# Performance work log

Hardware: AMD Instinct MI355X
Metric: run time of the kernel (lower is better)

The kernel has to match this reference:

```python
import jax, jax.numpy as jnp
import numpy as np

B, T, C = 2, 2048, 1024
H = 16
D = C // H  # head_size = 64
FF = 4 * C
EPS = 1e-5


def _layernorm(x, g, b):
    mu = jnp.mean(x, axis=-1, keepdims=True)
    var = jnp.var(x, axis=-1, keepdims=True)
    return (x - mu) * jax.lax.rsqrt(var + EPS) * g + b


def setup_inputs() -> dict:
    key = jax.random.key(0)
    ks = jax.random.split(key, 12)
    s_in = 1.0 / np.sqrt(C)
    s_ff = 1.0 / np.sqrt(FF)
    return {
        "x": jax.random.normal(ks[0], (B, T, C), jnp.float32),
        "Wq": jax.random.uniform(ks[1], (H, C, D), jnp.float32, -s_in, s_in),
        "Wk": jax.random.uniform(ks[2], (H, C, D), jnp.float32, -s_in, s_in),
        "Wv": jax.random.uniform(ks[3], (H, C, D), jnp.float32, -s_in, s_in),
        "Wo": jax.random.uniform(ks[4], (C, C), jnp.float32, -s_in, s_in),
        "bo": jax.random.uniform(ks[5], (C,), jnp.float32, -s_in, s_in),
        "W1": jax.random.uniform(ks[6], (C, FF), jnp.float32, -s_in, s_in),
        "b1": jax.random.uniform(ks[7], (FF,), jnp.float32, -s_in, s_in),
        "W2": jax.random.uniform(ks[8], (FF, C), jnp.float32, -s_ff, s_ff),
        "b2": jax.random.uniform(ks[9], (C,), jnp.float32, -s_ff, s_ff),
        "g1": jnp.ones((C,), jnp.float32),
        "be1": jnp.zeros((C,), jnp.float32),
        "g2": jnp.ones((C,), jnp.float32),
        "be2": jnp.zeros((C,), jnp.float32),
    }


def reference(x, Wq, Wk, Wv, Wo, bo, W1, b1, W2, b2, g1, be1, g2, be2):
    h = _layernorm(x, g1, be1)
    # per-head projections (no bias), vectorized over heads
    q = jnp.einsum("btc,hcd->bhtd", h, Wq)
    k = jnp.einsum("btc,hcd->bhtd", h, Wk)
    v = jnp.einsum("btc,hcd->bhtd", h, Wv)
    # NOTE: original scales by n_embd**-0.5 (C, not head_size) -- faithful
    scores = jnp.einsum("bhtd,bhsd->bhts", q, k) * (C ** -0.5)
    causal = jnp.tril(jnp.ones((T, T), bool))
    scores = jnp.where(causal, scores, -jnp.inf)
    att = jax.nn.softmax(scores, axis=-1)
    out = jnp.einsum("bhts,bhsd->bhtd", att, v)
    out = out.transpose(0, 2, 1, 3).reshape(B, T, C)  # concat heads
    x = out @ Wo + bo + x  # attn residual (dropout=0 -> identity)
    h2 = _layernorm(x, g2, be2)
    ff = jax.nn.relu(h2 @ W1 + b1) @ W2 + b2
    return x + ff
```

## Files before the change

kernel.cpp:

```cpp
#include <hip/hip_runtime.h>
#include <stdint.h>

typedef unsigned short ushort_t;
typedef __attribute__((ext_vector_type(8))) short bf16x8;
typedef __attribute__((ext_vector_type(4))) float f32x4;

__device__ __forceinline__ unsigned short f2b(float f) {
  unsigned u = __float_as_uint(f);
  u += 0x7fffu + ((u >> 16) & 1u);
  return (unsigned short)(u >> 16);
}

__device__ __forceinline__ void async16(const void* g, void* l) {
  __builtin_amdgcn_global_load_lds(
      (const __attribute__((address_space(1))) void*)g,
      (__attribute__((address_space(3))) void*)l, 16, 0, 0);
}

__global__ __launch_bounds__(256) void ln_kernel(
    const float* __restrict__ x, const float* __restrict__ g,
    const float* __restrict__ be, ushort_t* __restrict__ out) {
  const int C = 1024;
  int row = blockIdx.x;
  const float4* xr = (const float4*)(x + (size_t)row * C);
  int tid = threadIdx.x;
  float4 v = xr[tid];
  float s = v.x + v.y + v.z + v.w;
  float sq = v.x * v.x + v.y * v.y + v.z * v.z + v.w * v.w;
  #pragma unroll
  for (int off = 32; off > 0; off >>= 1) {
    s += __shfl_xor(s, off);
    sq += __shfl_xor(sq, off);
  }
  __shared__ float ss[4], ssq[4];
  int wv = tid >> 6;
  if ((tid & 63) == 0) { ss[wv] = s; ssq[wv] = sq; }
  __syncthreads();
  s = ss[0] + ss[1] + ss[2] + ss[3];
  sq = ssq[0] + ssq[1] + ssq[2] + ssq[3];
  float mu = s * (1.f / C);
  float var = sq * (1.f / C) - mu * mu;
  float rs = rsqrtf(var + 1e-5f);
  float4 gv = ((const float4*)g)[tid];
  float4 bv = ((const float4*)be)[tid];
  ushort4 o;
  o.x = f2b((v.x - mu) * rs * gv.x + bv.x);
  o.y = f2b((v.y - mu) * rs * gv.y + bv.y);
  o.z = f2b((v.z - mu) * rs * gv.z + bv.z);
  o.w = f2b((v.w - mu) * rs * gv.w + bv.w);
  ((ushort4*)(out + (size_t)row * C))[tid] = o;
}

__global__ __launch_bounds__(256) void reduce2_kernel(
    const float* __restrict__ p0, const float* __restrict__ p1,
    const float* __restrict__ bias, const float* __restrict__ resid,
    float* __restrict__ out) {
  int idx = blockIdx.x * 256 + threadIdx.x;
  float4 a = ((const float4*)p0)[idx];
  float4 b = ((const float4*)p1)[idx];
  float4 r = ((const float4*)resid)[idx];
  float4 bi = ((const float4*)bias)[idx & 255];
  float4 o;
  o.x = a.x + b.x + r.x + bi.x;
  o.y = a.y + b.y + r.y + bi.y;
  o.z = a.z + b.z + r.z + bi.z;
  o.w = a.w + b.w + r.w + bi.w;
  ((float4*)out)[idx] = o;
}

__global__ __launch_bounds__(256) void transpose_cast_kernel(
    const float* __restrict__ in, ushort_t* __restrict__ out, int R, int Cin) {
  __shared__ float tile[32][33];
  int bz = blockIdx.z;
  in += (size_t)bz * R * Cin;
  out += (size_t)bz * R * Cin;
  int c0 = blockIdx.x * 32, r0 = blockIdx.y * 32;
  int tx = threadIdx.x, ty = threadIdx.y;
  #pragma unroll
  for (int i = 0; i < 4; i++)
    tile[ty + 8 * i][tx] = in[(size_t)(r0 + ty + 8 * i) * Cin + c0 + tx];
  __syncthreads();
  #pragma unroll
  for (int i = 0; i < 4; i++)
    out[(size_t)(c0 + ty + 8 * i) * R + r0 + tx] = f2b(tile[tx][ty + 8 * i]);
}

__global__ __launch_bounds__(256) void transpose_v_kernel(
    const ushort_t* __restrict__ qkv, ushort_t* __restrict__ vt) {
  __shared__ ushort_t tile[32][33];
  int bh = blockIdx.z;
  int b = bh >> 4, h = bh & 15;
  int d0 = blockIdx.x * 32, t0 = blockIdx.y * 32;
  int tx = threadIdx.x, ty = threadIdx.y;
  #pragma unroll
  for (int i = 0; i < 4; i++)
    tile[ty + 8 * i][tx] =
        qkv[(size_t)(b * 2048 + t0 + ty + 8 * i) * 3072 + 2048 + h * 64 + d0 + tx];
  __syncthreads();
  #pragma unroll
  for (int i = 0; i < 4; i++)
    vt[(size_t)(bh * 64 + d0 + ty + 8 * i) * 2048 + t0 + tx] = tile[tx][ty + 8 * i];
}

template <int BN, int N, int K, int FLAGS, int SK>
__global__ __launch_bounds__(256, 3) void gemm_bt_kernel(
    const ushort_t* __restrict__ A, const ushort_t* __restrict__ Bt,
    const float* __restrict__ bias, const float* __restrict__ resid,
    void* __restrict__ outv, float* __restrict__ pp0, float* __restrict__ pp1) {
  constexpr int KS = K / SK;
  __shared__ ushort_t Als[2][128 * 32];
  __shared__ ushort_t Bls[2][128 * 32];
  int tid = threadIdx.x, w = tid >> 6, lane = tid & 63, quad = lane >> 4, l16 = lane & 15;
  int fid = blockIdx.x;
  int bn_low = (fid >> 3) & 7;
  int meta = (fid & 7) | ((fid >> 6) << 3);
  int bm = meta & 31;
  int high = meta >> 5;
  int bn, zz;
  if constexpr (SK > 1) { zz = high; bn = bn_low; }
  else { zz = 0; bn = bn_low + 8 * high; }
  int bn0 = bn * 128, bm0 = bm * 128;
  int koff = (SK > 1) ? zz * KS : 0;
  int wm = (w >> 1) * 64, wn = (w & 1) * 64;
  f32x4 acc[4][4];
  #pragma unroll
  for (int i = 0; i < 4; i++)
    #pragma unroll
    for (int j = 0; j < 4; j++) acc[i][j] = f32x4{0.f, 0.f, 0.f, 0.f};
  const ushort_t* Ag = A + (size_t)bm0 * K + koff;
  const ushort_t* Bg = Bt + (size_t)bn0 * K + koff;
  int lr = lane >> 2, lco = (lane & 3) * 8;
  auto stage = [&](int k0, int bi) {
    async16(Ag + (size_t)(w * 32 + lr) * K + k0 + lco, &Als[bi][w * 1024]);
    async16(Ag + (size_t)(w * 32 + 16 + lr) * K + k0 + lco, &Als[bi][w * 1024 + 512]);
    async16(Bg + (size_t)(w * 32 + lr) * K + k0 + lco, &Bls[bi][w * 1024]);
    async16(Bg + (size_t)(w * 32 + 16 + lr) * K + k0 + lco, &Bls[bi][w * 1024 + 512]);
  };
  stage(0, 0);
  int s = 0;
  for (int k0 = 0; k0 < KS; k0 += 32, s ^= 1) {
    __syncthreads();
    if (k0 + 32 < KS) stage(k0 + 32, s ^ 1);
    bf16x8 af[4], bf[4];
    #pragma unroll
    for (int i = 0; i < 4; i++)
      af[i] = *(const bf16x8*)&Als[s][(wm + i * 16 + l16) * 32 + quad * 8];
    #pragma unroll
    for (int j = 0; j < 4; j++)
      bf[j] = *(const bf16x8*)&Bls[s][(wn + j * 16 + l16) * 32 + quad * 8];
    #pragma unroll
    for (int i = 0; i < 4; i++)
      #pragma unroll
      for (int j = 0; j < 4; j++)
        acc[i][j] = __builtin_amdgcn_mfma_f32_16x16x32_bf16(af[i], bf[j], acc[i][j], 0, 0, 0);
  }
  float* pdst = nullptr;
  if constexpr (SK > 1) pdst = zz ? pp1 : pp0;
  #pragma unroll
  for (int i = 0; i < 4; i++)
    #pragma unroll
    for (int j = 0; j < 4; j++)
      #pragma unroll
      for (int r = 0; r < 4; r++) {
        int row = bm0 + wm + i * 16 + quad * 4 + r;
        int col = bn0 + wn + j * 16 + l16;
        float v = acc[i][j][r];
        if constexpr (SK > 1) {
          pdst[(size_t)row * N + col] = v;
        } else {
          if constexpr (FLAGS & 4) v += bias[col];
          if constexpr (FLAGS & 8) v += resid[(size_t)row * N + col];
          if constexpr (FLAGS & 1) v = fmaxf(v, 0.f);
          if constexpr ((FLAGS & 2) != 0)
            ((ushort_t*)outv)[(size_t)row * N + col] = f2b(v);
          else
            ((float*)outv)[(size_t)row * N + col] = v;
        }
      }
}

__global__ __launch_bounds__(256, 4) void attn_kernel(
    const ushort_t* __restrict__ qkv, const ushort_t* __restrict__ vt,
    ushort_t* __restrict__ out) {
  const int T = 2048, CC = 3072;
  __shared__ ushort_t Kls[2][2 * 64 * 32];
  __shared__ ushort_t Vls[2][2 * 64 * 32];
  int fid = blockIdx.x;
  int bh = (fid & 7) * 4 + ((fid >> 3) & 3);
  int qb = 31 - (fid >> 5);
  int b = bh >> 4, h = bh & 15;
  int q0 = qb * 64;
  int tid = threadIdx.x, w = tid >> 6, lane = tid & 63, quad = lane >> 4, l16 = lane & 15;
  int srow = w * 16 + (lane >> 2);
  int sco = (lane & 3) * 8;
  const ushort_t* kg = qkv + (size_t)(b * T + srow) * CC + 1024 + h * 64 + sco;
  const ushort_t* vg = vt + (size_t)(bh * 64 + srow) * T + sco;
  int q0s = q0 + w * 16;
  int trow = q0s + l16;
  const ushort_t* qp = qkv + (size_t)(b * T + trow) * CC + h * 64 + quad * 8;
  bf16x8 aq[2] = { *(const bf16x8*)qp, *(const bf16x8*)(qp + 32) };
  f32x4 O[4];
  #pragma unroll
  for (int i = 0; i < 4; i++) O[i] = f32x4{0.f, 0.f, 0.f, 0.f};
  float mrun = -1e30f, lrun = 0.f;
  const float ksc = 0.03125f * 1.44269504f;
  int src0 = (quad & 1) * 32 + l16;
  int src1 = src0 + 16;
  bool hiq = quad >= 2;
  auto stage = [&](int kb, int bi) {
    int s0 = kb * 64;
    async16(kg + (size_t)s0 * CC, &Kls[bi][w * 512]);
    async16(kg + (size_t)s0 * CC + 32, &Kls[bi][2048 + w * 512]);
    async16(vg + s0, &Vls[bi][w * 512]);
    async16(vg + s0 + 32, &Vls[bi][2048 + w * 512]);
  };
  stage(0, 0);
  for (int kb = 0; kb <= qb; kb++) {
    __syncthreads();
    if (kb < qb) stage(kb + 1, (kb + 1) & 1);
    int bi = kb & 1;
    int s0 = kb * 64;
    bf16x8 kfr[4][2], vfr[4][2];
    #pragma unroll
    for (int t = 0; t < 4; t++)
      #pragma unroll
      for (int ks = 0; ks < 2; ks++) {
        kfr[t][ks] = *(const bf16x8*)&Kls[bi][(ks * 64 + t * 16 + l16) * 32 + quad * 8];
        vfr[t][ks] = *(const bf16x8*)&Vls[bi][(ks * 64 + t * 16 + l16) * 32 + quad * 8];
      }
    f32x4 st[4];
    #pragma unroll
    for (int t = 0; t < 4; t++) {
      st[t] = f32x4{0.f, 0.f, 0.f, 0.f};
      #pragma unroll
      for (int ks = 0; ks < 2; ks++)
        st[t] = __builtin_amdgcn_mfma_f32_16x16x32_bf16(kfr[t][ks], aq[ks], st[t], 0, 0, 0);
    }
    float sv[4][4];
    float vmax = -1e30f;
    if (kb == qb) {
      #pragma unroll
      for (int t = 0; t < 4; t++)
        #pragma unroll
        for (int r = 0; r < 4; r++) {
          float sc = st[t][r] * ksc;
          int scol = s0 + t * 16 + quad * 4 + r;
          if (scol > trow) sc = -1e30f;
          sv[t][r] = sc;
          vmax = fmaxf(vmax, sc);
        }
    } else {
      #pragma unroll
      for (int t = 0; t < 4; t++)
        #pragma unroll
        for (int r = 0; r < 4; r++) {
          float sc = st[t][r] * ksc;
          sv[t][r] = sc;
          vmax = fmaxf(vmax, sc);
        }
    }
    vmax = fmaxf(vmax, __shfl_xor(vmax, 16));
    vmax = fmaxf(vmax, __shfl_xor(vmax, 32));
    float mnew = fmaxf(mrun, vmax);
    float alpha = __builtin_amdgcn_exp2f(mrun - mnew);
    mrun = mnew;
    float psum = 0.f;
    int pk[4][2];
    #pragma unroll
    for (int t = 0; t < 4; t++) {
      float p0 = __builtin_amdgcn_exp2f(sv[t][0] - mnew);
      float p1 = __builtin_amdgcn_exp2f(sv[t][1] - mnew);
      float p2 = __builtin_amdgcn_exp2f(sv[t][2] - mnew);
      float p3 = __builtin_amdgcn_exp2f(sv[t][3] - mnew);
      psum += (p0 + p1) + (p2 + p3);
      pk[t][0] = (int)((unsigned)f2b(p0) | ((unsigned)f2b(p1) << 16));
      pk[t][1] = (int)((unsigned)f2b(p2) | ((unsigned)f2b(p3) << 16));
    }
    psum += __shfl_xor(psum, 16);
    psum += __shfl_xor(psum, 32);
    lrun = lrun * alpha + psum;
    #pragma unroll
    for (int dt = 0; dt < 4; dt++) O[dt] *= alpha;
    #pragma unroll
    for (int g32 = 0; g32 < 2; g32++) {
      int t0 = 2 * g32, t1 = t0 + 1;
      int a0 = __shfl(pk[t0][0], src0), b0 = __shfl(pk[t1][0], src0);
      int a1 = __shfl(pk[t0][1], src0), b1 = __shfl(pk[t1][1], src0);
      int a2 = __shfl(pk[t0][0], src1), b2 = __shfl(pk[t1][0], src1);
      int a3 = __shfl(pk[t0][1], src1), b3 = __shfl(pk[t1][1], src1);
      union { int4 i; bf16x8 h; } u;
      u.i.x = hiq ? b0 : a0;
      u.i.y = hiq ? b1 : a1;
      u.i.z = hiq ? b2 : a2;
      u.i.w = hiq ? b3 : a3;
      #pragma unroll
      for (int dt = 0; dt < 4; dt++)
        O[dt] = __builtin_amdgcn_mfma_f32_16x16x32_bf16(vfr[dt][g32], u.h, O[dt], 0, 0, 0);
    }
  }
  float inv = 1.f / lrun;
  #pragma unroll
  for (int dt = 0; dt < 4; dt++) {
    ushort4 o;
    unsigned short* op = (unsigned short*)&o;
    #pragma unroll
    for (int r = 0; r < 4; r++) op[r] = f2b(O[dt][r] * inv);
    *(ushort4*)&out[(size_t)(b * T + trow) * 1024 + h * 64 + dt * 16 + quad * 4] = o;
  }
}

extern "C" void kernel_launch(void* const* d_in, const int* in_sizes, int n_in,
                              void* d_out, int out_size, void* d_ws, size_t ws_size,
                              hipStream_t stream) {
  const int B = 2, T = 2048, C = 1024, H = 16, D = 64, FF = 4096;
  const int M = B * T;
  const float* x   = (const float*)d_in[0];
  const float* Wq  = (const float*)d_in[1];
  const float* Wk  = (const float*)d_in[2];
  const float* Wv  = (const float*)d_in[3];
  const float* Wo  = (const float*)d_in[4];
  const float* bo  = (const float*)d_in[5];
  const float* W1  = (const float*)d_in[6];
  const float* b1  = (const float*)d_in[7];
  const float* W2  = (const float*)d_in[8];
  const float* b2  = (const float*)d_in[9];
  const float* g1  = (const float*)d_in[10];
  const float* be1 = (const float*)d_in[11];
  const float* g2  = (const float*)d_in[12];
  const float* be2 = (const float*)d_in[13];
  float* out = (float*)d_out;

  char* ws = (char*)d_ws;
  size_t off = 0;
  auto alloc = [&](size_t bytes) {
    void* p = ws + off;
    off += (bytes + 255) & ~(size_t)255;
    return p;
  };
  ushort_t* qkvt = (ushort_t*)alloc((size_t)3 * C * C * 2);
  ushort_t* wot  = (ushort_t*)alloc((size_t)C * C * 2);
  ushort_t* w1t  = (ushort_t*)alloc((size_t)FF * C * 2);
  ushort_t* w2t  = (ushort_t*)alloc((size_t)C * FF * 2);
  ushort_t* hbuf = (ushort_t*)alloc((size_t)M * C * 2);
  ushort_t* big  = (ushort_t*)alloc((size_t)M * FF * 2);
  ushort_t* vtb  = (ushort_t*)alloc((size_t)M * C * 2);
  ushort_t* aout = (ushort_t*)alloc((size_t)M * C * 2);
  float*    x2   = (float*)alloc((size_t)M * C * 4);
  float* pf0 = (float*)vtb;
  float* pf1 = (float*)qkvt;

  dim3 tb(32, 8);
  transpose_cast_kernel<<<dim3(D / 32, C / 32, H), tb, 0, stream>>>(Wq, qkvt, C, D);
  transpose_cast_kernel<<<dim3(D / 32, C / 32, H), tb, 0, stream>>>(Wk, qkvt + (size_t)C * C, C, D);
  transpose_cast_kernel<<<dim3(D / 32, C / 32, H), tb, 0, stream>>>(Wv, qkvt + (size_t)2 * C * C, C, D);
  transpose_cast_kernel<<<dim3(C / 32, C / 32, 1), tb, 0, stream>>>(Wo, wot, C, C);
  transpose_cast_kernel<<<dim3(FF / 32, C / 32, 1), tb, 0, stream>>>(W1, w1t, C, FF);
  transpose_cast_kernel<<<dim3(C / 32, FF / 32, 1), tb, 0, stream>>>(W2, w2t, FF, C);
  ln_kernel<<<M, 256, 0, stream>>>(x, g1, be1, hbuf);
  gemm_bt_kernel<24, 3072, 1024, 2, 1><<<768, 256, 0, stream>>>(
      hbuf, qkvt, nullptr, nullptr, big, nullptr, nullptr);
  transpose_v_kernel<<<dim3(2, T / 32, B * H), tb, 0, stream>>>(big, vtb);
  attn_kernel<<<1024, 256, 0, stream>>>(big, vtb, aout);
  gemm_bt_kernel<8, 1024, 1024, 4 | 8, 1><<<256, 256, 0, stream>>>(
      aout, wot, bo, x, x2, nullptr, nullptr);
  ln_kernel<<<M, 256, 0, stream>>>(x2, g2, be2, hbuf);
  gemm_bt_kernel<32, 4096, 1024, 1 | 2 | 4, 1><<<1024, 256, 0, stream>>>(
      hbuf, w1t, b1, nullptr, big, nullptr, nullptr);
  gemm_bt_kernel<8, 1024, 4096, 0, 2><<<512, 256, 0, stream>>>(
      big, w2t, nullptr, nullptr, nullptr, pf0, pf1);
  reduce2_kernel<<<M * C / 1024, 256, 0, stream>>>(pf0, pf1, b2, x2, out);
}
```

Before: 365.1 us.

## Add 256x256-tile 8-wave GEMM kernel for QKV and FFN1 projections

Introduces a new GEMM kernel with 256x256 output tiles, 512 threads (8 waves, each computing 128x64), double-buffered LDS with async global-to-LDS loads, split A/B staging interleaved with MFMA phases, and setprio around MFMA bursts. It replaces the previous GEMM for the QKV projection (192 blocks) and the FFN first layer (256 blocks). The larger tiles raise arithmetic intensity and cut global/LDS traffic per FLOP. In exchange the grid shrinks to roughly one wave of blocks on the 256 CUs, which risks tail imbalance and higher register pressure.

```diff
diff --git a/kernel.cpp b/kernel.cpp
--- a/kernel.cpp
+++ b/kernel.cpp
@@ -179,6 +179,148 @@
       }
 }
 
+template <int N, int K, int FLAGS, int SK>
+__global__ __launch_bounds__(512, 2) void gemm256_kernel(
+    const ushort_t* __restrict__ A, const ushort_t* __restrict__ Bt,
+    const float* __restrict__ bias, const float* __restrict__ resid,
+    void* __restrict__ outv, float* __restrict__ pp0, float* __restrict__ pp1) {
+  constexpr int M = 4096;
+  constexpr int NBM = M / 256;
+  constexpr int NBN = N / 256;
+  constexpr int KS = K / SK;
+  constexpr int NT = KS / 32;
+  constexpr int NWG = NBM * NBN * SK;
+  __shared__ __align__(16) ushort_t Als[2][256 * 32];
+  __shared__ __align__(16) ushort_t Bls[2][256 * 32];
+  int tid = threadIdx.x, w = tid >> 6, lane = tid & 63;
+  int quad = lane >> 4, l16 = lane & 15;
+  int wm = w >> 2, wn = w & 3;
+  int bid = blockIdx.x;
+  int swz = (bid & 7) * (NWG / 8) + (bid >> 3);
+  int z = 0;
+  if constexpr (SK > 1) { z = swz / (NBM * NBN); swz -= z * (NBM * NBN); }
+  int bm = swz / NBN, bn = swz - bm * NBN;
+  int bm0 = bm * 256, bn0 = bn * 256;
+  int koff = z * KS;
+  int lr = lane >> 2;
+  int kc = (lane & 3) ^ (lr & 3);
+  const ushort_t* Abase = A + (size_t)(bm0 + w * 16 + lr) * K + koff + kc * 8;
+  int brow = (w >> 1) * 64 + (w & 1) * 16;
+  const ushort_t* Bbase = Bt + (size_t)(bn0 + brow + lr) * K + koff + kc * 8;
+  int rofsA = (wm * 128 + l16) * 32 + (quad ^ (l16 & 3)) * 8;
+  int rofsB = (wn * 64 + l16) * 32 + (quad ^ (l16 & 3)) * 8;
+  f32x4 acc[8][4];
+  #pragma unroll
+  for (int mi = 0; mi < 8; mi++)
+    #pragma unroll
+    for (int ni = 0; ni < 4; ni++) acc[mi][ni] = f32x4{0.f, 0.f, 0.f, 0.f};
+
+  auto stageA = [&](int t, int p) {
+    const ushort_t* s2 = Abase + t * 32;
+    async16(s2, &Als[p][w * 512]);
+    async16(s2 + (size_t)128 * K, &Als[p][4096 + w * 512]);
+  };
+  auto stageB = [&](int t, int p, int hi) {
+    async16(Bbase + (size_t)(hi * 32) * K + t * 32, &Bls[p][(brow + hi * 32) * 32]);
+  };
+
+  stageA(0, 0);
+  stageB(0, 0, 0);
+  stageB(0, 0, 1);
+  asm volatile("s_waitcnt vmcnt(1)" ::: "memory");
+  __builtin_amdgcn_s_barrier();
+
+  int p = 0;
+  bf16x8 af[8], bfr[4];
+  for (int t = 0; t < NT - 1; ++t, p ^= 1) {
+    #pragma unroll
+    for (int mi = 0; mi < 8; mi++) af[mi] = *(const bf16x8*)&Als[p][rofsA + mi * 512];
+    bfr[0] = *(const bf16x8*)&Bls[p][rofsB];
+    bfr[1] = *(const bf16x8*)&Bls[p][rofsB + 512];
+    stageA(t + 1, p ^ 1);
+    __builtin_amdgcn_s_barrier();
+    asm volatile("s_waitcnt lgkmcnt(0)" ::: "memory");
+    __builtin_amdgcn_sched_barrier(0);
+    __builtin_amdgcn_s_setprio(1);
+    #pragma unroll
+    for (int mi = 0; mi < 8; mi++) {
+      acc[mi][0] = __builtin_amdgcn_mfma_f32_16x16x32_bf16(af[mi], bfr[0], acc[mi][0], 0, 0, 0);
+      acc[mi][1] = __builtin_amdgcn_mfma_f32_16x16x32_bf16(af[mi], bfr[1], acc[mi][1], 0, 0, 0);
+    }
+    __builtin_amdgcn_s_setprio(0);
+    asm volatile("s_waitcnt vmcnt(2)" ::: "memory");
+    __builtin_amdgcn_s_barrier();
+    bfr[2] = *(const bf16x8*)&Bls[p][rofsB + 1024];
+    bfr[3] = *(const bf16x8*)&Bls[p][rofsB + 1536];
+    stageB(t + 1, p ^ 1, 0);
+    stageB(t + 1, p ^ 1, 1);
+    __builtin_amdgcn_s_barrier();
+    asm volatile("s_waitcnt lgkmcnt(0)" ::: "memory");
+    __builtin_amdgcn_sched_barrier(0);
+    __builtin_amdgcn_s_setprio(1);
+    #pragma unroll
+    for (int mi = 0; mi < 8; mi++) {
+      acc[mi][2] = __builtin_amdgcn_mfma_f32_16x16x32_bf16(af[mi], bfr[2], acc[mi][2], 0, 0, 0);
+      acc[mi][3] = __builtin_amdgcn_mfma_f32_16x16x32_bf16(af[mi], bfr[3], acc[mi][3], 0, 0, 0);
+    }
+    __builtin_amdgcn_s_setprio(0);
+    asm volatile("s_waitcnt vmcnt(1)" ::: "memory");
+    __builtin_amdgcn_s_barrier();
+  }
+  {
+    #pragma unroll
+    for (int mi = 0; mi < 8; mi++) af[mi] = *(const bf16x8*)&Als[p][rofsA + mi * 512];
+    bfr[0] = *(const bf16x8*)&Bls[p][rofsB];
+    bfr[1] = *(const bf16x8*)&Bls[p][rofsB + 512];
+    __builtin_amdgcn_s_barrier();
+    asm volatile("s_waitcnt lgkmcnt(0)" ::: "memory");
+    __builtin_amdgcn_sched_barrier(0);
+    __builtin_amdgcn_s_setprio(1);
+    #pragma unroll
+    for (int mi = 0; mi < 8; mi++) {
+      acc[mi][0] = __builtin_amdgcn_mfma_f32_16x16x32_bf16(af[mi], bfr[0], acc[mi][0], 0, 0, 0);
+      acc[mi][1] = __builtin_amdgcn_mfma_f32_16x16x32_bf16(af[mi], bfr[1], acc[mi][1], 0, 0, 0);
+    }
+    __builtin_amdgcn_s_setprio(0);
+    asm volatile("s_waitcnt vmcnt(0)" ::: "memory");
+    __builtin_amdgcn_s_barrier();
+    bfr[2] = *(const bf16x8*)&Bls[p][rofsB + 1024];
+    bfr[3] = *(const bf16x8*)&Bls[p][rofsB + 1536];
+    asm volatile("s_waitcnt lgkmcnt(0)" ::: "memory");
+    __builtin_amdgcn_sched_barrier(0);
+    __builtin_amdgcn_s_setprio(1);
+    #pragma unroll
+    for (int mi = 0; mi < 8; mi++) {
+      acc[mi][2] = __builtin_amdgcn_mfma_f32_16x16x32_bf16(af[mi], bfr[2], acc[mi][2], 0, 0, 0);
+      acc[mi][3] = __builtin_amdgcn_mfma_f32_16x16x32_bf16(af[mi], bfr[3], acc[mi][3], 0, 0, 0);
+    }
+    __builtin_amdgcn_s_setprio(0);
+  }
+  float* pdst = nullptr;
+  if constexpr (SK > 1) pdst = z ? pp1 : pp0;
+  #pragma unroll
+  for (int mi = 0; mi < 8; mi++)
+    #pragma unroll
+    for (int ni = 0; ni < 4; ni++)
+      #pragma unroll
+      for (int r = 0; r < 4; r++) {
+        int row = bm0 + wm * 128 + mi * 16 + quad * 4 + r;
+        int col = bn0 + wn * 64 + ni * 16 + l16;
+        float v = acc[mi][ni][r];
+        if constexpr (SK > 1) {
+          pdst[(size_t)row * N + col] = v;
+        } else {
+          if constexpr (FLAGS & 4) v += bias[col];
+          if constexpr (FLAGS & 8) v += resid[(size_t)row * N + col];
+          if constexpr (FLAGS & 1) v = fmaxf(v, 0.f);
+          if constexpr ((FLAGS & 2) != 0)
+            ((ushort_t*)outv)[(size_t)row * N + col] = f2b(v);
+          else
+            ((float*)outv)[(size_t)row * N + col] = v;
+        }
+      }
+}
+
 __global__ __launch_bounds__(256, 4) void attn_kernel(
     const ushort_t* __restrict__ qkv, const ushort_t* __restrict__ vt,
     ushort_t* __restrict__ out) {
@@ -357,14 +499,14 @@
   transpose_cast_kernel<<<dim3(FF / 32, C / 32, 1), tb, 0, stream>>>(W1, w1t, C, FF);
   transpose_cast_kernel<<<dim3(C / 32, FF / 32, 1), tb, 0, stream>>>(W2, w2t, FF, C);
   ln_kernel<<<M, 256, 0, stream>>>(x, g1, be1, hbuf);
-  gemm_bt_kernel<24, 3072, 1024, 2, 1><<<768, 256, 0, stream>>>(
+  gemm256_kernel<3072, 1024, 2, 1><<<192, 512, 0, stream>>>(
       hbuf, qkvt, nullptr, nullptr, big, nullptr, nullptr);
   transpose_v_kernel<<<dim3(2, T / 32, B * H), tb, 0, stream>>>(big, vtb);
   attn_kernel<<<1024, 256, 0, stream>>>(big, vtb, aout);
   gemm_bt_kernel<8, 1024, 1024, 4 | 8, 1><<<256, 256, 0, stream>>>(
       aout, wot, bo, x, x2, nullptr, nullptr);
   ln_kernel<<<M, 256, 0, stream>>>(x2, g2, be2, hbuf);
-  gemm_bt_kernel<32, 4096, 1024, 1 | 2 | 4, 1><<<1024, 256, 0, stream>>>(
+  gemm256_kernel<4096, 1024, 1 | 2 | 4, 1><<<256, 512, 0, stream>>>(
       hbuf, w1t, b1, nullptr, big, nullptr, nullptr);
   gemm_bt_kernel<8, 1024, 4096, 0, 2><<<512, 256, 0, stream>>>(
       big, w2t, nullptr, nullptr, nullptr, pf0, pf1);
```

Result: slower. 376.5 us (+3.1%).
